# Kernel optimization log

Measured on AMD Instinct MI355X. Metric: run time of the kernel, lower is better.

Reference implementation:

```python
import jax, jax.numpy as jnp
import numpy as np

H = 2048
NUM_K = 16
NUM_V = 32
DK = 128
DV = 128
KSZ = 4
KEY_DIM = NUM_K * DK      # 2048
VALUE_DIM = NUM_V * DV    # 4096
CONV_DIM = 2 * KEY_DIM + VALUE_DIM  # 8192
EPS = 1e-6
VPK = NUM_V // NUM_K      # 2


def _l2norm(x, eps=1e-6):
    return x * jax.lax.rsqrt(jnp.sum(x * x, axis=-1, keepdims=True) + eps)


def setup_inputs() -> dict:
    key = jax.random.key(0)
    ks = jax.random.split(key, 12)
    s = 0.02
    return {
        "hidden_in": jax.random.normal(ks[0], (1, 1, H), jnp.float32),
        "conv_state": jax.random.normal(ks[1], (1, CONV_DIM, KSZ), jnp.float32),
        "rec_state": jax.random.normal(ks[2], (1, NUM_V, DK, DV), jnp.float32) * 0.1,
        "conv_w": jax.random.normal(ks[3], (CONV_DIM, KSZ), jnp.float32) * s,
        "in_proj_qkv_w": jax.random.normal(ks[4], (CONV_DIM, H), jnp.float32) * s,
        "in_proj_z_w": jax.random.normal(ks[5], (VALUE_DIM, H), jnp.float32) * s,
        "in_proj_b_w": jax.random.normal(ks[6], (NUM_V, H), jnp.float32) * s,
        "in_proj_a_w": jax.random.normal(ks[7], (NUM_V, H), jnp.float32) * s,
        "out_proj_w": jax.random.normal(ks[8], (H, VALUE_DIM), jnp.float32) * s,
        "dt_bias": jax.random.normal(ks[9], (NUM_V,), jnp.float32) * 0.1,
        "A_log": jax.random.normal(ks[10], (NUM_V,), jnp.float32) * 0.1,
        "norm_w": jnp.ones((DV,), jnp.float32),
    }


def reference(hidden_in, conv_state, rec_state, conv_w, in_proj_qkv_w,
              in_proj_z_w, in_proj_b_w, in_proj_a_w, out_proj_w,
              dt_bias, A_log, norm_w):
    # ---- projections (B=1, T=1) ----
    h = hidden_in[:, 0, :]                                   # (1, H)
    mixed_qkv = jnp.einsum('bh,ch->bc', h, in_proj_qkv_w)    # (1, CONV_DIM)
    z = jnp.einsum('bh,vh->bv', h, in_proj_z_w)              # (1, VALUE_DIM)
    b = jnp.einsum('bh,nh->bn', h, in_proj_b_w)              # (1, NUM_V)
    a = jnp.einsum('bh,nh->bn', h, in_proj_a_w)              # (1, NUM_V)

    # ---- causal conv1d update (shift state, append new token) ----
    w = jnp.concatenate([conv_state, mixed_qkv[:, :, None]], axis=-1)  # (1, C, K+1)
    new_conv_state = w[:, :, 1:]                                       # (1, C, K)
    conv_out = jax.nn.silu(jnp.sum(new_conv_state * conv_w[None], axis=-1))  # (1, C)

    # ---- split heads ----
    q = conv_out[:, :KEY_DIM].reshape(1, NUM_K, DK)
    k = conv_out[:, KEY_DIM:2 * KEY_DIM].reshape(1, NUM_K, DK)
    v = conv_out[:, 2 * KEY_DIM:].reshape(1, NUM_V, DV)
    # repeat_interleave key heads to match value heads (GQA-style)
    q = jnp.repeat(q, VPK, axis=1)                           # (1, NUM_V, DK)
    k = jnp.repeat(k, VPK, axis=1)

    q_ = _l2norm(q) * (1.0 / np.sqrt(DK))
    k_ = _l2norm(k)

    # ---- gating ----
    beta = jax.nn.sigmoid(b)                                  # (1, NUM_V)
    g = -jnp.exp(A_log) * jax.nn.softplus(a + dt_bias)        # (1, NUM_V)
    g_exp = jnp.exp(g)

    # ---- gated delta-rule recurrent update ----
    rec = rec_state * g_exp[:, :, None, None]                 # (1, NUM_V, DK, DV)
    kv_mem = jnp.einsum('bhkv,bhk->bhv', rec, k_)             # (1, NUM_V, DV)
    delta = (v - kv_mem) * beta[:, :, None]
    rec = rec + k_[:, :, :, None] * delta[:, :, None, :]
    core = jnp.einsum('bhkv,bhk->bhv', rec, q_)               # (1, NUM_V, DV)

    # ---- gated RMSNorm per value head ----
    x = core.reshape(-1, DV)
    zf = z.reshape(-1, DV)
    var = jnp.mean(x * x, axis=-1, keepdims=True)
    xn = (x * jax.lax.rsqrt(var + EPS)) * norm_w
    out = xn * jax.nn.silu(zf)                                # (NUM_V, DV)

    hidden_out = jnp.einsum('bv,hv->bh', out.reshape(1, VALUE_DIM), out_proj_w)
    hidden_out = hidden_out.reshape(1, 1, H)
    return hidden_out, new_conv_state, rec
```

## Files before the change

### kernel.cpp

```cpp
#include <hip/hip_runtime.h>
#include <math.h>

#define H_DIM 2048
#define NUM_K 16
#define NUM_V 32
#define DK 128
#define DV 128
#define KSZ 4
#define KEY_DIM 2048
#define VALUE_DIM 4096
#define CONV_DIM 8192

#define WS_QKV   0
#define WS_Z     8192
#define WS_B     12288
#define WS_A     12320
#define WS_OUT   20544

__device__ __forceinline__ float wave_reduce_sum(float v) {
#pragma unroll
    for (int off = 32; off > 0; off >>= 1) v += __shfl_down(v, off, 64);
    return v;
}

__global__ void proj_kernel(const float* __restrict__ h,
                            const float* __restrict__ qkv_w,
                            const float* __restrict__ z_w,
                            const float* __restrict__ b_w,
                            const float* __restrict__ a_w,
                            float* __restrict__ ws) {
    const int R = CONV_DIM + VALUE_DIM + 2 * NUM_V;
    int wave = (blockIdx.x * blockDim.x + threadIdx.x) >> 6;
    int lane = threadIdx.x & 63;
    if (wave >= R) return;

    const float* row;
    float* dst;
    if (wave < CONV_DIM) {
        row = qkv_w + (size_t)wave * H_DIM;
        dst = ws + WS_QKV + wave;
    } else if (wave < CONV_DIM + VALUE_DIM) {
        int r = wave - CONV_DIM;
        row = z_w + (size_t)r * H_DIM;
        dst = ws + WS_Z + r;
    } else if (wave < CONV_DIM + VALUE_DIM + NUM_V) {
        int r = wave - CONV_DIM - VALUE_DIM;
        row = b_w + (size_t)r * H_DIM;
        dst = ws + WS_B + r;
    } else {
        int r = wave - CONV_DIM - VALUE_DIM - NUM_V;
        row = a_w + (size_t)r * H_DIM;
        dst = ws + WS_A + r;
    }

    const float4* row4 = (const float4*)row;
    const float4* h4 = (const float4*)h;
    float acc = 0.f;
#pragma unroll
    for (int i = 0; i < H_DIM / 256; ++i) {
        float4 w4 = row4[lane + 64 * i];
        float4 hv = h4[lane + 64 * i];
        acc += w4.x * hv.x + w4.y * hv.y + w4.z * hv.z + w4.w * hv.w;
    }
    acc = wave_reduce_sum(acc);
    if (lane == 0) *dst = acc;
}

__global__ __launch_bounds__(512) void head_kernel(
        const float* __restrict__ conv_state,
        const float* __restrict__ conv_w,
        float* __restrict__ ws,
        const float* __restrict__ rec_in,
        const float* __restrict__ dt_bias,
        const float* __restrict__ A_log,
        const float* __restrict__ norm_w,
        float* __restrict__ new_conv_state,
        float* __restrict__ rec_out) {
    __shared__ float qc[DK];
    __shared__ float kc[DK];
    __shared__ float vc[DV];
    __shared__ float delta_lds[DV];
    __shared__ float part[16][DV];
    __shared__ float red[4];

    const int n = blockIdx.x;
    const int sh = n >> 1;
    const int t = threadIdx.x;
    const int lane = t & 63;

    if (t < 384) {
        int slice = t >> 7;
        int j = t & 127;
        int c;
        if (slice == 0)      c = sh * DK + j;
        else if (slice == 1) c = KEY_DIM + sh * DK + j;
        else                 c = 2 * KEY_DIM + n * DV + j;
        float4 cs = ((const float4*)conv_state)[c];
        float4 w  = ((const float4*)conv_w)[c];
        float mq  = ws[WS_QKV + c];
        float pre = cs.y * w.x + cs.z * w.y + cs.w * w.z + mq * w.w;
        float so  = pre / (1.f + expf(-pre));
        if (slice == 0)      qc[j] = so;
        else if (slice == 1) kc[j] = so;
        else                 vc[j] = so;
        float4 ns; ns.x = cs.y; ns.y = cs.z; ns.z = cs.w; ns.w = mq;
        ((float4*)new_conv_state)[c] = ns;
    }
    __syncthreads();

    if (t < 64) {
        float s = qc[t] * qc[t] + qc[t + 64] * qc[t + 64];
        s = wave_reduce_sum(s);
        if (lane == 0) red[0] = s;
    } else if (t < 128) {
        int j = t - 64;
        float s = kc[j] * kc[j] + kc[j + 64] * kc[j + 64];
        s = wave_reduce_sum(s);
        if (lane == 0) red[1] = s;
    }
    __syncthreads();
    {
        float qin = rsqrtf(red[0] + 1e-6f) * 0.08838834764831845f;
        float kin = rsqrtf(red[1] + 1e-6f);
        if (t < 128) {
            qc[t] *= qin;
            kc[t] *= kin;
        }
    }

    float bb = ws[WS_B + n];
    float aa = ws[WS_A + n];
    float beta = 1.f / (1.f + expf(-bb));
    float x = aa + dt_bias[n];
    float sp = (x > 20.f) ? x : log1pf(expf(x));
    float gexp = expf(-expf(A_log[n]) * sp);
    __syncthreads();

    const float4* rn4 = (const float4*)(rec_in + (size_t)n * DK * DV);
    float4* ro4 = (float4*)(rec_out + (size_t)n * DK * DV);
    const int cg = t & 31;
    const int ch = t >> 5;

    {
        float4 kv = {0.f, 0.f, 0.f, 0.f};
#pragma unroll
        for (int j = 0; j < 8; ++j) {
            int k = ch * 8 + j;
            float4 r = rn4[k * 32 + cg];
            float kk = kc[k];
            kv.x += r.x * kk; kv.y += r.y * kk; kv.z += r.z * kk; kv.w += r.w * kk;
        }
        ((float4*)part[ch])[cg] = kv;
    }
    __syncthreads();
    if (t < DV) {
        float kv = 0.f;
#pragma unroll
        for (int c = 0; c < 16; ++c) kv += part[c][t];
        kv *= gexp;
        delta_lds[t] = (vc[t] - kv) * beta;
    }
    __syncthreads();

    {
        float4 d4 = ((const float4*)delta_lds)[cg];
        float4 core = {0.f, 0.f, 0.f, 0.f};
#pragma unroll
        for (int j = 0; j < 8; ++j) {
            int k = ch * 8 + j;
            float4 r = rn4[k * 32 + cg];
            float kk = kc[k];
            float4 val;
            val.x = r.x * gexp + kk * d4.x;
            val.y = r.y * gexp + kk * d4.y;
            val.z = r.z * gexp + kk * d4.z;
            val.w = r.w * gexp + kk * d4.w;
            ro4[k * 32 + cg] = val;
            float qq = qc[k];
            core.x += val.x * qq; core.y += val.y * qq;
            core.z += val.z * qq; core.w += val.w * qq;
        }
        ((float4*)part[ch])[cg] = core;
    }
    __syncthreads();

    if (t < DV) {
        float core = 0.f;
#pragma unroll
        for (int c = 0; c < 16; ++c) core += part[c][t];
        float s = wave_reduce_sum(core * core);
        if (lane == 0) red[2 + (t >> 6)] = s;
        vc[t] = core;
    }
    __syncthreads();
    if (t < DV) {
        float core = vc[t];
        float var = (red[2] + red[3]) * (1.f / DV);
        float xn = core * rsqrtf(var + 1e-6f) * norm_w[t];
        float zv = ws[WS_Z + n * DV + t];
        float silz = zv / (1.f + expf(-zv));
        ws[WS_OUT + n * DV + t] = xn * silz;
    }
}

__global__ void outproj_kernel(const float* __restrict__ ws,
                               const float* __restrict__ out_proj_w,
                               float* __restrict__ hidden_out) {
    int wave = (blockIdx.x * blockDim.x + threadIdx.x) >> 6;
    int lane = threadIdx.x & 63;
    if (wave >= H_DIM) return;
    const float4* row4 = (const float4*)(out_proj_w + (size_t)wave * VALUE_DIM);
    const float4* o4 = (const float4*)(ws + WS_OUT);
    float acc = 0.f;
#pragma unroll
    for (int i = 0; i < VALUE_DIM / 256; ++i) {
        float4 w4 = row4[lane + 64 * i];
        float4 ov = o4[lane + 64 * i];
        acc += w4.x * ov.x + w4.y * ov.y + w4.z * ov.z + w4.w * ov.w;
    }
    acc = wave_reduce_sum(acc);
    if (lane == 0) hidden_out[wave] = acc;
}

extern "C" void kernel_launch(void* const* d_in, const int* in_sizes, int n_in,
                              void* d_out, int out_size, void* d_ws, size_t ws_size,
                              hipStream_t stream) {
    const float* h          = (const float*)d_in[0];
    const float* conv_state = (const float*)d_in[1];
    const float* rec_in     = (const float*)d_in[2];
    const float* conv_w     = (const float*)d_in[3];
    const float* qkv_w      = (const float*)d_in[4];
    const float* z_w        = (const float*)d_in[5];
    const float* b_w        = (const float*)d_in[6];
    const float* a_w        = (const float*)d_in[7];
    const float* out_proj_w = (const float*)d_in[8];
    const float* dt_bias    = (const float*)d_in[9];
    const float* A_log      = (const float*)d_in[10];
    const float* norm_w     = (const float*)d_in[11];

    float* out = (float*)d_out;
    float* hidden_out = out;
    float* new_conv   = out + H_DIM;
    float* rec_out    = out + H_DIM + CONV_DIM * KSZ;
    float* ws = (float*)d_ws;

    proj_kernel<<<3088, 256, 0, stream>>>(h, qkv_w, z_w, b_w, a_w, ws);
    head_kernel<<<32, 512, 0, stream>>>(conv_state, conv_w, ws, rec_in,
                                        dt_bias, A_log, norm_w, new_conv, rec_out);
    outproj_kernel<<<512, 256, 0, stream>>>(ws, out_proj_w, hidden_out);
}
```

Baseline: 32.81 us.

## Move z projection into head kernel blocks and fuse SiLU gating into out-projection

The z projection (4096 rows of in_proj_z_w) moves out of the first projection kernel. Extra blocks in the head kernel now compute it alongside the 32 recurrent-head blocks, so that weight stream overlaps the mostly idle head stage. The head kernel drops to 256 threads per block and writes only the normalized core. The SiLU(z) gating is now applied in the out-projection kernel, which stages the gated vector in LDS per block. The cost is that all 512 out-projection blocks recompute the 4096-element gating redundantly.

```diff
diff --git a/kernel.cpp b/kernel.cpp
--- a/kernel.cpp
+++ b/kernel.cpp
@@ -2,7 +2,6 @@
 #include <math.h>
 
 #define H_DIM 2048
-#define NUM_K 16
 #define NUM_V 32
 #define DK 128
 #define DV 128
@@ -15,7 +14,7 @@
 #define WS_Z     8192
 #define WS_B     12288
 #define WS_A     12320
-#define WS_OUT   20544
+#define WS_XN    12352
 
 __device__ __forceinline__ float wave_reduce_sum(float v) {
 #pragma unroll
@@ -25,11 +24,10 @@
 
 __global__ void proj_kernel(const float* __restrict__ h,
                             const float* __restrict__ qkv_w,
-                            const float* __restrict__ z_w,
                             const float* __restrict__ b_w,
                             const float* __restrict__ a_w,
                             float* __restrict__ ws) {
-    const int R = CONV_DIM + VALUE_DIM + 2 * NUM_V;
+    const int R = CONV_DIM + 2 * NUM_V;
     int wave = (blockIdx.x * blockDim.x + threadIdx.x) >> 6;
     int lane = threadIdx.x & 63;
     if (wave >= R) return;
@@ -39,16 +37,12 @@
     if (wave < CONV_DIM) {
         row = qkv_w + (size_t)wave * H_DIM;
         dst = ws + WS_QKV + wave;
-    } else if (wave < CONV_DIM + VALUE_DIM) {
+    } else if (wave < CONV_DIM + NUM_V) {
         int r = wave - CONV_DIM;
-        row = z_w + (size_t)r * H_DIM;
-        dst = ws + WS_Z + r;
-    } else if (wave < CONV_DIM + VALUE_DIM + NUM_V) {
-        int r = wave - CONV_DIM - VALUE_DIM;
         row = b_w + (size_t)r * H_DIM;
         dst = ws + WS_B + r;
     } else {
-        int r = wave - CONV_DIM - VALUE_DIM - NUM_V;
+        int r = wave - CONV_DIM - NUM_V;
         row = a_w + (size_t)r * H_DIM;
         dst = ws + WS_A + r;
     }
@@ -57,7 +51,7 @@
     const float4* h4 = (const float4*)h;
     float acc = 0.f;
 #pragma unroll
-    for (int i = 0; i < H_DIM / 256; ++i) {
+    for (int i = 0; i < 8; ++i) {
         float4 w4 = row4[lane + 64 * i];
         float4 hv = h4[lane + 64 * i];
         acc += w4.x * hv.x + w4.y * hv.y + w4.z * hv.z + w4.w * hv.w;
@@ -66,9 +60,11 @@
     if (lane == 0) *dst = acc;
 }
 
-__global__ __launch_bounds__(512) void head_kernel(
+__global__ __launch_bounds__(256) void mid_kernel(
+        const float* __restrict__ h,
         const float* __restrict__ conv_state,
         const float* __restrict__ conv_w,
+        const float* __restrict__ z_w,
         float* __restrict__ ws,
         const float* __restrict__ rec_in,
         const float* __restrict__ dt_bias,
@@ -76,30 +72,49 @@
         const float* __restrict__ norm_w,
         float* __restrict__ new_conv_state,
         float* __restrict__ rec_out) {
-    __shared__ float qc[DK];
-    __shared__ float kc[DK];
-    __shared__ float vc[DV];
-    __shared__ float delta_lds[DV];
-    __shared__ float part[16][DV];
+    const int t = threadIdx.x;
+    const int lane = t & 63;
+    const int w = t >> 6;
+
+    if (blockIdx.x >= 32) {
+        int zb = blockIdx.x - 32;
+        const float4* h4 = (const float4*)h;
+#pragma unroll
+        for (int rr = 0; rr < 2; ++rr) {
+            int r = zb * 4 + w + rr * 2048;
+            const float4* r4 = (const float4*)(z_w + (size_t)r * H_DIM);
+            float acc = 0.f;
+#pragma unroll
+            for (int i = 0; i < 8; ++i) {
+                float4 w4 = r4[lane + 64 * i];
+                float4 hv = h4[lane + 64 * i];
+                acc += w4.x * hv.x + w4.y * hv.y + w4.z * hv.z + w4.w * hv.w;
+            }
+            acc = wave_reduce_sum(acc);
+            if (lane == 0) ws[WS_Z + r] = acc;
+        }
+        return;
+    }
+
+    __shared__ float qc[DK], kc[DK], vc[DV], dl[DV];
+    __shared__ float part[8][DV];
     __shared__ float red[4];
 
     const int n = blockIdx.x;
     const int sh = n >> 1;
-    const int t = threadIdx.x;
-    const int lane = t & 63;
-
-    if (t < 384) {
-        int slice = t >> 7;
-        int j = t & 127;
+
+    for (int idx = t; idx < 384; idx += 256) {
+        int slice = idx >> 7;
+        int j = idx & 127;
         int c;
         if (slice == 0)      c = sh * DK + j;
         else if (slice == 1) c = KEY_DIM + sh * DK + j;
         else                 c = 2 * KEY_DIM + n * DV + j;
         float4 cs = ((const float4*)conv_state)[c];
-        float4 w  = ((const float4*)conv_w)[c];
-        float mq  = ws[WS_QKV + c];
-        float pre = cs.y * w.x + cs.z * w.y + cs.w * w.z + mq * w.w;
-        float so  = pre / (1.f + expf(-pre));
+        float4 cw = ((const float4*)conv_w)[c];
+        float mq = ws[WS_QKV + c];
+        float pre = cs.y * cw.x + cs.z * cw.y + cs.w * cw.z + mq * cw.w;
+        float so = pre / (1.f + expf(-pre));
         if (slice == 0)      qc[j] = so;
         else if (slice == 1) kc[j] = so;
         else                 vc[j] = so;
@@ -119,107 +134,119 @@
         if (lane == 0) red[1] = s;
     }
     __syncthreads();
-    {
+    if (t < 128) {
         float qin = rsqrtf(red[0] + 1e-6f) * 0.08838834764831845f;
         float kin = rsqrtf(red[1] + 1e-6f);
-        if (t < 128) {
-            qc[t] *= qin;
-            kc[t] *= kin;
-        }
+        qc[t] *= qin;
+        kc[t] *= kin;
     }
 
     float bb = ws[WS_B + n];
     float aa = ws[WS_A + n];
     float beta = 1.f / (1.f + expf(-bb));
-    float x = aa + dt_bias[n];
-    float sp = (x > 20.f) ? x : log1pf(expf(x));
+    float xx = aa + dt_bias[n];
+    float sp = (xx > 20.f) ? xx : log1pf(expf(xx));
     float gexp = expf(-expf(A_log[n]) * sp);
     __syncthreads();
 
     const float4* rn4 = (const float4*)(rec_in + (size_t)n * DK * DV);
     float4* ro4 = (float4*)(rec_out + (size_t)n * DK * DV);
-    const int cg = t & 31;
-    const int ch = t >> 5;
+    const int cgp = t & 31;
+    const int chp = t >> 5;
 
     {
         float4 kv = {0.f, 0.f, 0.f, 0.f};
 #pragma unroll
-        for (int j = 0; j < 8; ++j) {
-            int k = ch * 8 + j;
-            float4 r = rn4[k * 32 + cg];
+        for (int j = 0; j < 16; ++j) {
+            int k = chp * 16 + j;
+            float4 r = rn4[k * 32 + cgp];
             float kk = kc[k];
             kv.x += r.x * kk; kv.y += r.y * kk; kv.z += r.z * kk; kv.w += r.w * kk;
         }
-        ((float4*)part[ch])[cg] = kv;
+        ((float4*)part[chp])[cgp] = kv;
     }
     __syncthreads();
     if (t < DV) {
-        float kv = 0.f;
-#pragma unroll
-        for (int c = 0; c < 16; ++c) kv += part[c][t];
-        kv *= gexp;
-        delta_lds[t] = (vc[t] - kv) * beta;
+        float s = 0.f;
+#pragma unroll
+        for (int c = 0; c < 8; ++c) s += part[c][t];
+        s *= gexp;
+        dl[t] = (vc[t] - s) * beta;
     }
     __syncthreads();
 
     {
-        float4 d4 = ((const float4*)delta_lds)[cg];
+        float4 d4 = ((const float4*)dl)[cgp];
         float4 core = {0.f, 0.f, 0.f, 0.f};
 #pragma unroll
-        for (int j = 0; j < 8; ++j) {
-            int k = ch * 8 + j;
-            float4 r = rn4[k * 32 + cg];
+        for (int j = 0; j < 16; ++j) {
+            int k = chp * 16 + j;
+            float4 r = rn4[k * 32 + cgp];
             float kk = kc[k];
+            float qq = qc[k];
             float4 val;
             val.x = r.x * gexp + kk * d4.x;
             val.y = r.y * gexp + kk * d4.y;
             val.z = r.z * gexp + kk * d4.z;
             val.w = r.w * gexp + kk * d4.w;
-            ro4[k * 32 + cg] = val;
-            float qq = qc[k];
+            ro4[k * 32 + cgp] = val;
             core.x += val.x * qq; core.y += val.y * qq;
             core.z += val.z * qq; core.w += val.w * qq;
         }
-        ((float4*)part[ch])[cg] = core;
-    }
-    __syncthreads();
-
+        ((float4*)part[chp])[cgp] = core;
+    }
+    __syncthreads();
     if (t < DV) {
-        float core = 0.f;
-#pragma unroll
-        for (int c = 0; c < 16; ++c) core += part[c][t];
-        float s = wave_reduce_sum(core * core);
+        float c = 0.f;
+#pragma unroll
+        for (int cc = 0; cc < 8; ++cc) c += part[cc][t];
+        float s = wave_reduce_sum(c * c);
         if (lane == 0) red[2 + (t >> 6)] = s;
-        vc[t] = core;
+        vc[t] = c;
     }
     __syncthreads();
     if (t < DV) {
-        float core = vc[t];
+        float c = vc[t];
         float var = (red[2] + red[3]) * (1.f / DV);
-        float xn = core * rsqrtf(var + 1e-6f) * norm_w[t];
-        float zv = ws[WS_Z + n * DV + t];
-        float silz = zv / (1.f + expf(-zv));
-        ws[WS_OUT + n * DV + t] = xn * silz;
-    }
-}
-
-__global__ void outproj_kernel(const float* __restrict__ ws,
-                               const float* __restrict__ out_proj_w,
-                               float* __restrict__ hidden_out) {
-    int wave = (blockIdx.x * blockDim.x + threadIdx.x) >> 6;
-    int lane = threadIdx.x & 63;
-    if (wave >= H_DIM) return;
-    const float4* row4 = (const float4*)(out_proj_w + (size_t)wave * VALUE_DIM);
-    const float4* o4 = (const float4*)(ws + WS_OUT);
+        ws[WS_XN + n * DV + t] = c * rsqrtf(var + 1e-6f) * norm_w[t];
+    }
+}
+
+__global__ __launch_bounds__(256) void outproj_kernel(
+        const float* __restrict__ ws,
+        const float* __restrict__ out_proj_w,
+        float* __restrict__ hidden_out) {
+    __shared__ float4 out_lds[VALUE_DIM / 4];
+
+    const int t = threadIdx.x;
+    const int lane = t & 63;
+    const int w = t >> 6;
+
+    const float4* xn4 = (const float4*)(ws + WS_XN);
+    const float4* z4 = (const float4*)(ws + WS_Z);
+    for (int i = t; i < VALUE_DIM / 4; i += 256) {
+        float4 x = xn4[i];
+        float4 z = z4[i];
+        float4 o;
+        o.x = x.x * (z.x / (1.f + expf(-z.x)));
+        o.y = x.y * (z.y / (1.f + expf(-z.y)));
+        o.z = x.z * (z.z / (1.f + expf(-z.z)));
+        o.w = x.w * (z.w / (1.f + expf(-z.w)));
+        out_lds[i] = o;
+    }
+    __syncthreads();
+
+    const int row = blockIdx.x * 4 + w;
+    const float4* r4 = (const float4*)(out_proj_w + (size_t)row * VALUE_DIM);
     float acc = 0.f;
 #pragma unroll
-    for (int i = 0; i < VALUE_DIM / 256; ++i) {
-        float4 w4 = row4[lane + 64 * i];
-        float4 ov = o4[lane + 64 * i];
+    for (int i = 0; i < 16; ++i) {
+        float4 w4 = r4[lane + 64 * i];
+        float4 ov = out_lds[lane + 64 * i];
         acc += w4.x * ov.x + w4.y * ov.y + w4.z * ov.z + w4.w * ov.w;
     }
     acc = wave_reduce_sum(acc);
-    if (lane == 0) hidden_out[wave] = acc;
+    if (lane == 0) hidden_out[row] = acc;
 }
 
 extern "C" void kernel_launch(void* const* d_in, const int* in_sizes, int n_in,
@@ -244,8 +271,8 @@
     float* rec_out    = out + H_DIM + CONV_DIM * KSZ;
     float* ws = (float*)d_ws;
 
-    proj_kernel<<<3088, 256, 0, stream>>>(h, qkv_w, z_w, b_w, a_w, ws);
-    head_kernel<<<32, 512, 0, stream>>>(conv_state, conv_w, ws, rec_in,
+    proj_kernel<<<2064, 256, 0, stream>>>(h, qkv_w, b_w, a_w, ws);
+    mid_kernel<<<544, 256, 0, stream>>>(h, conv_state, conv_w, z_w, ws, rec_in,
                                         dt_bias, A_log, norm_w, new_conv, rec_out);
     outproj_kernel<<<512, 256, 0, stream>>>(ws, out_proj_w, hidden_out);
 }
```

Measured after the change: 33.82 us. 1.03x slower.
